# Optimization experiments

Hardware: AMD Instinct MI355X
Metric: run time of the kernel (lower is better)

## Reference

```python
import jax, jax.numpy as jnp
import numpy as np
from jax.ops import segment_sum, segment_max

N_USERS = 50000
N_ITEMS = 30000
N_ENTITIES = 80000
D = 64
KG_HOPS = 2        # context_hops / KG_layers
LGCN_LAYERS = 2    # n_layers
TEMP = 0.2
N_KG_EDGES = 2_000_000
N_INTERACT = 1_000_000
N_ADJ = 2_000_000
EPS_PD = 1e-6      # torch PairwiseDistance default eps


def _normalize(x):
    # F.normalize(x, p=2, dim=-1)
    n = jnp.linalg.norm(x, axis=-1, keepdims=True)
    return x / jnp.clip(n, 1e-12)


def _spmm(rows, cols, vals, x, n_rows):
    # sparse (n_rows x k) @ dense (k x d) via gather + segment_sum
    return segment_sum(vals[:, None] * x[cols], rows, num_segments=n_rows)


def setup_inputs() -> dict:
    key = jax.random.key(0)
    ks = jax.random.split(key, 9)
    all_embed = jax.random.normal(ks[0], (N_USERS + N_ENTITIES, D), dtype=jnp.float32) * 0.1
    interact_vals = jax.random.uniform(ks[1], (N_INTERACT,), dtype=jnp.float32)
    adj_vals = jax.random.uniform(ks[2], (N_ADJ,), dtype=jnp.float32)
    edge_index = jax.random.randint(ks[3], (2, N_KG_EDGES), 0, N_ENTITIES, dtype=jnp.int32)
    edge_type = jax.random.randint(ks[4], (N_KG_EDGES,), 0, 32, dtype=jnp.int32)
    interact_rows = jnp.sort(jax.random.randint(ks[5], (N_INTERACT,), 0, N_USERS, dtype=jnp.int32))
    interact_cols = jax.random.randint(ks[6], (N_INTERACT,), 0, N_ITEMS, dtype=jnp.int32)
    adj_rows = jax.random.randint(ks[7], (N_ADJ,), 0, N_USERS + N_ITEMS, dtype=jnp.int32)
    adj_cols = jax.random.randint(ks[8], (N_ADJ,), 0, N_USERS + N_ITEMS, dtype=jnp.int32)
    return {
        "all_embed": all_embed,
        "interact_vals": interact_vals,
        "adj_vals": adj_vals,
        "edge_index": edge_index,
        "edge_type": edge_type,
        "interact_rows": interact_rows,
        "interact_cols": interact_cols,
        "adj_rows": adj_rows,
        "adj_cols": adj_cols,
    }


def _forward(all_embed, interact_vals, adj_vals, edge_index, interact_rows,
             interact_cols, adj_rows, adj_cols):
    user_emb = all_embed[:N_USERS]
    entity_emb = all_embed[N_USERS:]
    head, tail = edge_index[0], edge_index[1]

    u_res, e_res = user_emb, entity_emb
    u, e = user_emb, entity_emb
    ones = jnp.ones((head.shape[0],), dtype=entity_emb.dtype)
    cnt = jnp.clip(segment_sum(ones, head, num_segments=N_ENTITIES), 1.0)

    for _ in range(KG_HOPS):
        # scatter_mean KG aggregation: entity_agg[h] = mean over tails of edges with head h
        entity_agg = segment_sum(e[tail], head, num_segments=N_ENTITIES) / cnt[:, None]
        item_agg = entity_agg[:N_ITEMS]
        # user_mean = interact_map @ entity_agg[:n_items]
        user_mean = _spmm(interact_rows, interact_cols, interact_vals, item_agg, N_USERS)
        # pairwise L2 distance per interaction nnz
        diff = item_agg[interact_cols] - user_mean[interact_rows] + EPS_PD
        score = jnp.linalg.norm(diff, axis=-1) / TEMP
        # sparse softmax over rows (users)
        m = segment_max(score, interact_rows, num_segments=N_USERS)
        ex = jnp.exp(score - m[interact_rows])
        denom = segment_sum(ex, interact_rows, num_segments=N_USERS)
        att = ex / denom[interact_rows]
        # user_agg = sparse.mm(soft_score_mat, item_agg)
        user_agg = segment_sum(att[:, None] * item_agg[interact_cols],
                               interact_rows, num_segments=N_USERS)
        e = _normalize(entity_agg)
        u = _normalize(user_agg)
        e_res = e_res + e
        u_res = u_res + u

    # LightGCN over bipartite graph
    x = jnp.concatenate([u_res, e_res[:N_ITEMS]], axis=0)  # [n_users+n_items, D]
    acc = x
    for _ in range(LGCN_LAYERS):
        x = _spmm(adj_rows, adj_cols, adj_vals, x, N_USERS + N_ITEMS)
        acc = acc + x
    out = acc / float(LGCN_LAYERS + 1)
    return out[:N_USERS], out[N_USERS:]


def reference(all_embed, interact_vals, adj_vals, edge_index, edge_type,
              interact_rows, interact_cols, adj_rows, adj_cols):
    # edge_type is passed through the original forward but unused by Aggregator
    return _forward(all_embed, interact_vals, adj_vals, edge_index,
                    interact_rows, interact_cols, adj_rows, adj_cols)
```

## Files before the change

kernel.cpp:

```cpp
#include <hip/hip_runtime.h>
#include <math.h>

#define N_USERS 50000
#define N_ITEMS 30000
#define N_ENTITIES 80000
#define N_UI (N_USERS + N_ITEMS)
#define D 64
#define N_KG_EDGES 2000000
#define N_INTERACT 1000000
#define N_ADJ 2000000
#define INV_TEMP 5.0f
#define EPS_PD 1e-6f
#define SHIFT 7
#define NB 625
#define BKEYS 128
#define BMASK 127
#define EPB 8192
#define BIG 1024
#define GRID_EP 245
#define UH_GRID 12500
#define KG2_GRID 7500
#define CVT_GRID 1875

typedef _Float16 f16;

__device__ __forceinline__ float4 ld_h4(const f16* p) {
    struct h4 { f16 x, y, z, w; };
    h4 h = *(const h4*)p;
    return make_float4((float)h.x, (float)h.y, (float)h.z, (float)h.w);
}

__device__ __forceinline__ void st_h4(f16* p, float4 v) {
    struct h4 { f16 x, y, z, w; };
    h4 h = {(f16)v.x, (f16)v.y, (f16)v.z, (f16)v.w};
    *(h4*)p = h;
}

__global__ void bhist_plus(const int* __restrict__ kg_ei, const int* __restrict__ adj_r,
                           const int* __restrict__ irows, int* __restrict__ bcntK,
                           int* __restrict__ bcntA, int* __restrict__ rowstart) {
    __shared__ int h[NB];
    int bb = blockIdx.x;
    if (bb < 2 * GRID_EP) {
        bool kg = bb < GRID_EP;
        const int* keys = kg ? kg_ei : adj_r;
        int* bcnt = kg ? bcntK : bcntA;
        int blk = kg ? bb : bb - GRID_EP;
        int n = kg ? N_KG_EDGES : N_ADJ;
        for (int i = threadIdx.x; i < NB; i += BIG) h[i] = 0;
        __syncthreads();
        int e0 = blk * EPB, e1 = min(e0 + EPB, n);
        for (int e = e0 + (int)threadIdx.x; e < e1; e += BIG)
            atomicAdd(&h[keys[e] >> SHIFT], 1);
        __syncthreads();
        for (int i = threadIdx.x; i < NB; i += BIG)
            if (h[i]) atomicAdd(&bcnt[i], h[i]);
    } else {
        int r = (bb - 2 * GRID_EP) * BIG + threadIdx.x;
        if (r > N_USERS) return;
        int lo = 0, hi = N_INTERACT;
        while (lo < hi) {
            int mid = (lo + hi) >> 1;
            if (irows[mid] < r) lo = mid + 1; else hi = mid;
        }
        rowstart[r] = lo;
    }
}

__global__ void bscan_both(const int* __restrict__ cntK, int* __restrict__ boffK,
                           int* __restrict__ bcurK, const int* __restrict__ cntA,
                           int* __restrict__ boffA, int* __restrict__ bcurA) {
    __shared__ int wp[4];
    __shared__ int carry_s;
    const int* cnt = blockIdx.x ? cntA : cntK;
    int* boff = blockIdx.x ? boffA : boffK;
    int* bcur = blockIdx.x ? bcurA : bcurK;
    int lane = threadIdx.x & 63, wv = threadIdx.x >> 6;
    if (threadIdx.x == 0) { carry_s = 0; boff[0] = 0; }
    __syncthreads();
    for (int base = 0; base < NB; base += 256) {
        int i = base + (int)threadIdx.x;
        int v = (i < NB) ? cnt[i] : 0;
        int x = v;
        #pragma unroll
        for (int o = 1; o < 64; o <<= 1) {
            int t = __shfl_up(x, o, 64);
            if (lane >= o) x += t;
        }
        if (lane == 63) wp[wv] = x;
        __syncthreads();
        int add = carry_s;
        for (int j = 0; j < wv; ++j) add += wp[j];
        int incl = x + add;
        if (i < NB) { boff[i + 1] = incl; bcur[i] = incl - v; }
        __syncthreads();
        if (threadIdx.x == 255) carry_s = incl;
        __syncthreads();
    }
}

__global__ void binA_both(const int* __restrict__ kg_ei, int* __restrict__ bcurK,
                          int* __restrict__ kg_bin, const int* __restrict__ adj_r,
                          const int* __restrict__ adj_c, const float* __restrict__ adj_v,
                          int* __restrict__ bcurA, int2* __restrict__ rc) {
    __shared__ int hist[NB], base[NB];
    bool kg = blockIdx.x < GRID_EP;
    int blk = kg ? blockIdx.x : blockIdx.x - GRID_EP;
    int n = kg ? N_KG_EDGES : N_ADJ;
    int* bcur = kg ? bcurK : bcurA;
    const int* keys = kg ? kg_ei : adj_r;
    for (int i = threadIdx.x; i < NB; i += BIG) hist[i] = 0;
    __syncthreads();
    int e0 = blk * EPB;
    for (int i = threadIdx.x; i < EPB; i += BIG) {
        int e = e0 + i;
        if (e < n) atomicAdd(&hist[keys[e] >> SHIFT], 1);
    }
    __syncthreads();
    for (int b = threadIdx.x; b < NB; b += BIG)
        base[b] = hist[b] ? atomicAdd(&bcur[b], hist[b]) : 0;
    __syncthreads();
    for (int i = threadIdx.x; i < NB; i += BIG) hist[i] = 0;
    __syncthreads();
    for (int i = threadIdx.x; i < EPB; i += BIG) {
        int e = e0 + i;
        if (e >= n) continue;
        int k = keys[e];
        int b = k >> SHIFT;
        int slot = base[b] + atomicAdd(&hist[b], 1);
        if (kg) kg_bin[slot] = (kg_ei[n + e] << SHIFT) | (k & BMASK);
        else    rc[slot] = make_int2((adj_c[e] << SHIFT) | (k & BMASK),
                                     __float_as_int(adj_v[e]));
    }
}

__global__ void binC_both(const int* __restrict__ boffK, const int* __restrict__ kg_bin,
                          int* __restrict__ tails, int* __restrict__ rowptrK,
                          float* __restrict__ icnt, const int* __restrict__ boffA,
                          const int2* __restrict__ rc, int2* __restrict__ pair,
                          int* __restrict__ rowptrA) {
    __shared__ int cnt_s[BKEYS];
    __shared__ int cur_s[BKEYS];
    __shared__ int wp2[2];
    bool kg = blockIdx.x < NB;
    int b = kg ? blockIdx.x : blockIdx.x - NB;
    const int* boff = kg ? boffK : boffA;
    int k0 = b << SHIFT;
    int s = boff[b], t = boff[b + 1];
    if (threadIdx.x < BKEYS) cnt_s[threadIdx.x] = 0;
    __syncthreads();
    for (int i = s + (int)threadIdx.x; i < t; i += 256)
        atomicAdd(&cnt_s[(kg ? kg_bin[i] : rc[i].x) & BMASK], 1);
    __syncthreads();
    int lane = threadIdx.x & 63, wv = threadIdx.x >> 6;
    int v = (threadIdx.x < BKEYS) ? cnt_s[threadIdx.x] : 0;
    int x = v;
    #pragma unroll
    for (int o = 1; o < 64; o <<= 1) {
        int tt = __shfl_up(x, o, 64);
        if (lane >= o) x += tt;
    }
    if (threadIdx.x < BKEYS && lane == 63) wp2[wv] = x;
    __syncthreads();
    int add = (wv == 1) ? wp2[0] : 0;
    int excl = s + (x - v) + add;
    if (threadIdx.x < BKEYS) {
        cur_s[threadIdx.x] = excl;
        if (kg) {
            rowptrK[k0 + threadIdx.x] = excl;
            icnt[k0 + threadIdx.x] = 1.0f / fmaxf((float)v, 1.0f);
        } else {
            rowptrA[k0 + threadIdx.x] = excl;
        }
    }
    if (threadIdx.x == 0 && b == NB - 1) {
        if (kg) rowptrK[N_ENTITIES] = t; else rowptrA[N_UI] = t;
    }
    __syncthreads();
    if (kg) {
        for (int i = s + (int)threadIdx.x; i < t; i += 256) {
            int p = kg_bin[i];
            int slot = atomicAdd(&cur_s[p & BMASK], 1);
            tails[slot] = (unsigned)p >> SHIFT;
        }
    } else {
        for (int i = s + (int)threadIdx.x; i < t; i += 256) {
            int2 p = rc[i];
            int slot = atomicAdd(&cur_s[p.x & BMASK], 1);
            pair[slot] = make_int2((unsigned)p.x >> SHIFT, p.y);
        }
    }
}

template <bool FIRST>
__device__ __forceinline__ void kg_hop_body(
        int wid, const int* __restrict__ rowptr, const int* __restrict__ tails,
        const float* __restrict__ icnt, const float* __restrict__ Ain,
        float* __restrict__ Aout, float* __restrict__ ER,
        const float* __restrict__ ERI, float* __restrict__ snorm, int nrows) {
    int lane = threadIdx.x & 63;
    int g = lane >> 4, gl = lane & 15;
    if (wid >= nrows) return;
    int s = rowptr[wid], t = rowptr[wid + 1];
    float4 acc = {0.f, 0.f, 0.f, 0.f};
    for (int e = s + g; e < t; e += 16) {
        int e1 = e + 4, e2 = e + 8, e3 = e + 12;
        int c0 = tails[e];
        int c1 = (e1 < t) ? tails[e1] : 0;
        int c2 = (e2 < t) ? tails[e2] : 0;
        int c3 = (e3 < t) ? tails[e3] : 0;
        float4 r0 = *(const float4*)(Ain + (size_t)c0 * D + gl * 4);
        float4 r1 = {0.f, 0.f, 0.f, 0.f};
        float4 r2 = {0.f, 0.f, 0.f, 0.f};
        float4 r3 = {0.f, 0.f, 0.f, 0.f};
        if (e1 < t) r1 = *(const float4*)(Ain + (size_t)c1 * D + gl * 4);
        if (e2 < t) r2 = *(const float4*)(Ain + (size_t)c2 * D + gl * 4);
        if (e3 < t) r3 = *(const float4*)(Ain + (size_t)c3 * D + gl * 4);
        acc.x += (r0.x + r1.x) + (r2.x + r3.x);
        acc.y += (r0.y + r1.y) + (r2.y + r3.y);
        acc.z += (r0.z + r1.z) + (r2.z + r3.z);
        acc.w += (r0.w + r1.w) + (r2.w + r3.w);
    }
    acc.x += __shfl_xor(acc.x, 16, 64); acc.x += __shfl_xor(acc.x, 32, 64);
    acc.y += __shfl_xor(acc.y, 16, 64); acc.y += __shfl_xor(acc.y, 32, 64);
    acc.z += __shfl_xor(acc.z, 16, 64); acc.z += __shfl_xor(acc.z, 32, 64);
    acc.w += __shfl_xor(acc.w, 16, 64); acc.w += __shfl_xor(acc.w, 32, 64);
    float ss = acc.x * acc.x + acc.y * acc.y + acc.z * acc.z + acc.w * acc.w;
    ss += __shfl_xor(ss, 1, 64); ss += __shfl_xor(ss, 2, 64);
    ss += __shfl_xor(ss, 4, 64); ss += __shfl_xor(ss, 8, 64);
    float nrm = fmaxf(sqrtf(ss), 1e-12f);
    float inv = 1.0f / nrm;
    if (g == 0) {
        size_t o = (size_t)wid * D + gl * 4;
        float4 ev = {acc.x * inv, acc.y * inv, acc.z * inv, acc.w * inv};
        *(float4*)(Aout + o) = ev;
        if (wid < N_ITEMS) {
            float4 er = FIRST ? *(const float4*)(ERI + o) : *(const float4*)(ER + o);
            er.x += ev.x; er.y += ev.y; er.z += ev.z; er.w += ev.w;
            *(float4*)(ER + o) = er;
            if (gl == 0) snorm[wid] = nrm * icnt[wid];
        }
    }
}

template <bool FIRST>
__device__ __forceinline__ void user_hop_body(
        int wid, const float* __restrict__ E, const float* __restrict__ snorm,
        const int* __restrict__ rowstart, const int* __restrict__ cols,
        const float* __restrict__ vals, float* __restrict__ UR,
        const float* __restrict__ URI, f16* __restrict__ XHu) {
    int lane = threadIdx.x & 63;
    int g = lane >> 4, gl = lane & 15;
    if (wid >= N_USERS) return;
    int s = rowstart[wid], t = rowstart[wid + 1];

    float4 mean = {0.f, 0.f, 0.f, 0.f};
    #define UH_LOAD(K)                                                          \
        const int eP##K = s + g + 4 * K;                                        \
        const bool ok##K = eP##K < t;                                           \
        const int cP##K = ok##K ? cols[eP##K] : 0;                              \
        const float snP##K = ok##K ? snorm[cP##K] : 0.f;                        \
        const float vP##K = ok##K ? vals[eP##K] : 0.f;                          \
        float4 rP##K = {0.f, 0.f, 0.f, 0.f};                                    \
        if (ok##K) rP##K = *(const float4*)(E + (size_t)cP##K * D + gl * 4);
    UH_LOAD(0) UH_LOAD(1) UH_LOAD(2) UH_LOAD(3) UH_LOAD(4) UH_LOAD(5)
    #undef UH_LOAD
    #define UH_MEAN(K) {                                                        \
        float w = vP##K * snP##K;                                               \
        mean.x += w * rP##K.x; mean.y += w * rP##K.y;                           \
        mean.z += w * rP##K.z; mean.w += w * rP##K.w; }
    UH_MEAN(0) UH_MEAN(1) UH_MEAN(2) UH_MEAN(3) UH_MEAN(4) UH_MEAN(5)
    #undef UH_MEAN
    for (int e = s + g + 24; e < t; e += 4) {
        int c = cols[e];
        float w = vals[e] * snorm[c];
        float4 r = *(const float4*)(E + (size_t)c * D + gl * 4);
        mean.x += w * r.x; mean.y += w * r.y;
        mean.z += w * r.z; mean.w += w * r.w;
    }
    mean.x += __shfl_xor(mean.x, 16, 64); mean.x += __shfl_xor(mean.x, 32, 64);
    mean.y += __shfl_xor(mean.y, 16, 64); mean.y += __shfl_xor(mean.y, 32, 64);
    mean.z += __shfl_xor(mean.z, 16, 64); mean.z += __shfl_xor(mean.z, 32, 64);
    mean.w += __shfl_xor(mean.w, 16, 64); mean.w += __shfl_xor(mean.w, 32, 64);

    float m = -INFINITY, denom = 0.f;
    float4 acc = {0.f, 0.f, 0.f, 0.f};
    #define UH_SM(K) if (ok##K) {                                               \
        float4 il = {snP##K * rP##K.x, snP##K * rP##K.y,                        \
                     snP##K * rP##K.z, snP##K * rP##K.w};                       \
        float dx = il.x - mean.x + EPS_PD;                                      \
        float dy = il.y - mean.y + EPS_PD;                                      \
        float dz = il.z - mean.z + EPS_PD;                                      \
        float dw = il.w - mean.w + EPS_PD;                                      \
        float ssl = dx * dx + dy * dy + dz * dz + dw * dw;                      \
        ssl += __shfl_xor(ssl, 1, 64); ssl += __shfl_xor(ssl, 2, 64);           \
        ssl += __shfl_xor(ssl, 4, 64); ssl += __shfl_xor(ssl, 8, 64);           \
        float sc = sqrtf(ssl) * INV_TEMP;                                       \
        float m_new = fmaxf(m, sc);                                             \
        float scale = __expf(m - m_new);                                        \
        float ex = __expf(sc - m_new);                                          \
        denom = denom * scale + ex;                                             \
        acc.x = acc.x * scale + ex * il.x;                                      \
        acc.y = acc.y * scale + ex * il.y;                                      \
        acc.z = acc.z * scale + ex * il.z;                                      \
        acc.w = acc.w * scale + ex * il.w;                                      \
        m = m_new; }
    UH_SM(0) UH_SM(1) UH_SM(2) UH_SM(3) UH_SM(4) UH_SM(5)
    #undef UH_SM
    for (int e = s + g + 24; e < t; e += 4) {
        int c = cols[e];
        float sn = snorm[c];
        float4 r = *(const float4*)(E + (size_t)c * D + gl * 4);
        float4 il = {sn * r.x, sn * r.y, sn * r.z, sn * r.w};
        float dx = il.x - mean.x + EPS_PD;
        float dy = il.y - mean.y + EPS_PD;
        float dz = il.z - mean.z + EPS_PD;
        float dw = il.w - mean.w + EPS_PD;
        float ssl = dx * dx + dy * dy + dz * dz + dw * dw;
        ssl += __shfl_xor(ssl, 1, 64); ssl += __shfl_xor(ssl, 2, 64);
        ssl += __shfl_xor(ssl, 4, 64); ssl += __shfl_xor(ssl, 8, 64);
        float sc = sqrtf(ssl) * INV_TEMP;
        float m_new = fmaxf(m, sc);
        float scale = __expf(m - m_new);
        float ex = __expf(sc - m_new);
        denom = denom * scale + ex;
        acc.x = acc.x * scale + ex * il.x;
        acc.y = acc.y * scale + ex * il.y;
        acc.z = acc.z * scale + ex * il.z;
        acc.w = acc.w * scale + ex * il.w;
        m = m_new;
    }
    float mg = fmaxf(m, __shfl_xor(m, 16, 64));
    mg = fmaxf(mg, __shfl_xor(mg, 32, 64));
    float scl = __expf(fmaxf(m - mg, -88.0f));
    denom *= scl;
    acc.x *= scl; acc.y *= scl; acc.z *= scl; acc.w *= scl;
    denom += __shfl_xor(denom, 16, 64); denom += __shfl_xor(denom, 32, 64);
    acc.x += __shfl_xor(acc.x, 16, 64); acc.x += __shfl_xor(acc.x, 32, 64);
    acc.y += __shfl_xor(acc.y, 16, 64); acc.y += __shfl_xor(acc.y, 32, 64);
    acc.z += __shfl_xor(acc.z, 16, 64); acc.z += __shfl_xor(acc.z, 32, 64);
    acc.w += __shfl_xor(acc.w, 16, 64); acc.w += __shfl_xor(acc.w, 32, 64);
    float invd = denom > 0.f ? 1.0f / denom : 0.f;
    acc.x *= invd; acc.y *= invd; acc.z *= invd; acc.w *= invd;
    float ss = acc.x * acc.x + acc.y * acc.y + acc.z * acc.z + acc.w * acc.w;
    ss += __shfl_xor(ss, 1, 64); ss += __shfl_xor(ss, 2, 64);
    ss += __shfl_xor(ss, 4, 64); ss += __shfl_xor(ss, 8, 64);
    float inv = 1.0f / fmaxf(sqrtf(ss), 1e-12f);
    if (g == 0) {
        size_t o = (size_t)wid * D + gl * 4;
        float4 u = FIRST ? *(const float4*)(URI + o) : *(const float4*)(UR + o);
        u.x += acc.x * inv; u.y += acc.y * inv; u.z += acc.z * inv; u.w += acc.w * inv;
        *(float4*)(UR + o) = u;
        if (XHu) st_h4(XHu + o, u);
    }
}

__global__ void kg1_kernel(const int* __restrict__ rowptr, const int* __restrict__ tails,
                           const float* __restrict__ icnt, const float* __restrict__ Ain,
                           float* __restrict__ A1, float* __restrict__ ER,
                           const float* __restrict__ ERI, float* __restrict__ sn1) {
    int wid = (blockIdx.x * blockDim.x + threadIdx.x) >> 6;
    kg_hop_body<true>(wid, rowptr, tails, icnt, Ain, A1, ER, ERI, sn1, N_ENTITIES);
}

__global__ void mid_kernel(const float* __restrict__ A1, const float* __restrict__ sn1,
                           const int* __restrict__ rowstart, const int* __restrict__ cols,
                           const float* __restrict__ vals, float* __restrict__ UR,
                           const float* __restrict__ URI, const int* __restrict__ rowptr,
                           const int* __restrict__ tails, const float* __restrict__ icnt,
                           float* __restrict__ A0I, float* __restrict__ ER,
                           float* __restrict__ sn2) {
    if (blockIdx.x < UH_GRID) {
        int wid = (blockIdx.x * blockDim.x + threadIdx.x) >> 6;
        user_hop_body<true>(wid, A1, sn1, rowstart, cols, vals, UR, URI, nullptr);
    } else {
        int wid = (((blockIdx.x - UH_GRID) * blockDim.x) + threadIdx.x) >> 6;
        kg_hop_body<false>(wid, rowptr, tails, icnt, A1, A0I, ER, nullptr, sn2, N_ITEMS);
    }
}

__global__ void fin_kernel(const float* __restrict__ A0I, const float* __restrict__ sn2,
                           const int* __restrict__ rowstart, const int* __restrict__ cols,
                           const float* __restrict__ vals, float* __restrict__ UR,
                           f16* __restrict__ XH, const float* __restrict__ ER) {
    if (blockIdx.x < UH_GRID) {
        int wid = (blockIdx.x * blockDim.x + threadIdx.x) >> 6;
        user_hop_body<false>(wid, A0I, sn2, rowstart, cols, vals, UR, nullptr, XH);
    } else {
        int i = (blockIdx.x - UH_GRID) * blockDim.x + threadIdx.x;
        if (i < (N_ITEMS * D) / 4)
            st_h4(XH + (size_t)N_USERS * D + (size_t)i * 4,
                  *(const float4*)(ER + (size_t)i * 4));
    }
}

__device__ __forceinline__ const float* xrow32(const float* U, const float* I, int c) {
    return (c < N_USERS) ? (U + (size_t)c * D) : (I + (size_t)(c - N_USERS) * D);
}

template <int MODE>
__global__ void adj_spmm(const int* __restrict__ rowptr, const int2* __restrict__ pair,
                         const f16* __restrict__ X, const float* __restrict__ XAU,
                         const float* __restrict__ XAI, f16* __restrict__ Y,
                         float* __restrict__ out) {
    int wid = (blockIdx.x * blockDim.x + threadIdx.x) >> 6;
    int lane = threadIdx.x & 63;
    int g = lane >> 4, gl = lane & 15;
    if (wid >= N_UI) return;
    int s = rowptr[wid], t = rowptr[wid + 1];
    float4 acc = {0.f, 0.f, 0.f, 0.f};
    for (int e = s + g; e < t; e += 16) {
        int e1 = e + 4, e2 = e + 8, e3 = e + 12;
        int2 p0 = pair[e];
        int2 p1 = (e1 < t) ? pair[e1] : make_int2(0, 0);
        int2 p2 = (e2 < t) ? pair[e2] : make_int2(0, 0);
        int2 p3 = (e3 < t) ? pair[e3] : make_int2(0, 0);
        float4 r0 = ld_h4(X + (size_t)p0.x * D + gl * 4);
        float4 r1 = {0.f, 0.f, 0.f, 0.f};
        float4 r2 = {0.f, 0.f, 0.f, 0.f};
        float4 r3 = {0.f, 0.f, 0.f, 0.f};
        if (e1 < t) r1 = ld_h4(X + (size_t)p1.x * D + gl * 4);
        if (e2 < t) r2 = ld_h4(X + (size_t)p2.x * D + gl * 4);
        if (e3 < t) r3 = ld_h4(X + (size_t)p3.x * D + gl * 4);
        float v0 = __int_as_float(p0.y), v1 = __int_as_float(p1.y);
        float v2 = __int_as_float(p2.y), v3 = __int_as_float(p3.y);
        acc.x += (v0 * r0.x + v1 * r1.x) + (v2 * r2.x + v3 * r3.x);
        acc.y += (v0 * r0.y + v1 * r1.y) + (v2 * r2.y + v3 * r3.y);
        acc.z += (v0 * r0.z + v1 * r1.z) + (v2 * r2.z + v3 * r3.z);
        acc.w += (v0 * r0.w + v1 * r1.w) + (v2 * r2.w + v3 * r3.w);
    }
    acc.x += __shfl_xor(acc.x, 16, 64); acc.x += __shfl_xor(acc.x, 32, 64);
    acc.y += __shfl_xor(acc.y, 16, 64); acc.y += __shfl_xor(acc.y, 32, 64);
    acc.z += __shfl_xor(acc.z, 16, 64); acc.z += __shfl_xor(acc.z, 32, 64);
    acc.w += __shfl_xor(acc.w, 16, 64); acc.w += __shfl_xor(acc.w, 32, 64);
    if (g == 0) {
        size_t o = (size_t)wid * D + gl * 4;
        if (MODE == 0) {
            st_h4(Y + o, acc);
            const float4 xa = *(const float4*)(xrow32(XAU, XAI, wid) + gl * 4);
            float4 ov = {xa.x + acc.x, xa.y + acc.y, xa.z + acc.z, xa.w + acc.w};
            *(float4*)(out + o) = ov;
        } else {
            float4 ov = *(const float4*)(out + o);
            ov.x = (ov.x + acc.x) * (1.0f / 3.0f);
            ov.y = (ov.y + acc.y) * (1.0f / 3.0f);
            ov.z = (ov.z + acc.z) * (1.0f / 3.0f);
            ov.w = (ov.w + acc.w) * (1.0f / 3.0f);
            *(float4*)(out + o) = ov;
        }
    }
}

extern "C" void kernel_launch(void* const* d_in, const int* in_sizes, int n_in,
                              void* d_out, int out_size, void* d_ws, size_t ws_size,
                              hipStream_t stream) {
    const float* all_embed     = (const float*)d_in[0];
    const float* interact_vals = (const float*)d_in[1];
    const float* adj_vals      = (const float*)d_in[2];
    const int*   edge_index    = (const int*)d_in[3];
    const int*   interact_rows = (const int*)d_in[5];
    const int*   interact_cols = (const int*)d_in[6];
    const int*   adj_rows      = (const int*)d_in[7];
    const int*   adj_cols      = (const int*)d_in[8];
    float* out = (float*)d_out;

    const size_t usrN = (size_t)N_USERS * D;
    const size_t itmN = (size_t)N_ITEMS * D;
    const size_t entN = (size_t)N_ENTITIES * D;

    float* cur = (float*)d_ws;
    float* UR  = cur; cur += usrN;
    float* ER  = cur; cur += itmN;
    float* A0I = cur; cur += itmN;
    float* A1  = cur; cur += entN;
    int* KG_TAIL = (int*)cur; cur += N_KG_EDGES;
    int2* ADJ_PAIR = (int2*)cur; cur += 2 * (size_t)N_ADJ;
    float* ICNT   = cur; cur += N_ENTITIES;
    float* SNORM1 = cur; cur += N_ITEMS + 16;
    float* SNORM2 = cur; cur += N_ITEMS + 16;
    int* KG_ROWPTR  = (int*)cur;
    int* ADJ_ROWPTR = KG_ROWPTR + N_ENTITIES + 2;
    int* BCNT_K     = ADJ_ROWPTR + N_UI + 2;
    int* BCNT_A     = BCNT_K + NB;
    int* BOFF_K     = BCNT_A + NB;
    int* BOFF_A     = BOFF_K + NB + 1;
    int* BCUR_K     = BOFF_A + NB + 1;
    int* BCUR_A     = BCUR_K + NB;
    int* ROWSTART   = BCUR_A + NB;

    int*  KG_BIN = (int*)UR;
    int2* ADJ_RC = (int2*)A1;
    f16*  XH  = (f16*)A1;
    f16*  X1H = XH + (size_t)N_UI * D;

    hipMemsetAsync(BCNT_K, 0, 2 * NB * sizeof(int), stream);
    bhist_plus<<<2 * GRID_EP + 49, BIG, 0, stream>>>(edge_index, adj_rows, interact_rows,
                                                     BCNT_K, BCNT_A, ROWSTART);
    bscan_both<<<2, 256, 0, stream>>>(BCNT_K, BOFF_K, BCUR_K, BCNT_A, BOFF_A, BCUR_A);
    binA_both<<<2 * GRID_EP, BIG, 0, stream>>>(edge_index, BCUR_K, KG_BIN, adj_rows,
                                               adj_cols, adj_vals, BCUR_A, ADJ_RC);
    binC_both<<<2 * NB, 256, 0, stream>>>(BOFF_K, KG_BIN, KG_TAIL, KG_ROWPTR, ICNT,
                                          BOFF_A, ADJ_RC, ADJ_PAIR, ADJ_ROWPTR);

    kg1_kernel<<<N_ENTITIES / 4, 256, 0, stream>>>(KG_ROWPTR, KG_TAIL, ICNT,
                                                   all_embed + usrN, A1, ER,
                                                   all_embed + usrN, SNORM1);
    mid_kernel<<<UH_GRID + KG2_GRID, 256, 0, stream>>>(A1, SNORM1, ROWSTART,
                                                       interact_cols, interact_vals,
                                                       UR, all_embed, KG_ROWPTR, KG_TAIL,
                                                       ICNT, A0I, ER, SNORM2);
    fin_kernel<<<UH_GRID + CVT_GRID, 256, 0, stream>>>(A0I, SNORM2, ROWSTART,
                                                       interact_cols, interact_vals,
                                                       UR, XH, ER);

    adj_spmm<0><<<N_UI / 4, 256, 0, stream>>>(ADJ_ROWPTR, ADJ_PAIR, XH, UR, ER, X1H, out);
    adj_spmm<1><<<N_UI / 4, 256, 0, stream>>>(ADJ_ROWPTR, ADJ_PAIR, X1H, nullptr, nullptr,
                                              nullptr, out);
}
```

Before: 415.2 us.

## Overlap adjacency binning with KG hops, pack adj pairs, simplify softmax distance

The adjacency binning passes move out of the standalone bin kernels and into kg1 and mid as extra blocks, so they run alongside the KG and user hop work. Adjacency (col, val) pairs are packed into one 32-bit word holding a 17-bit column and a 15-bit fp16 value with the sign bit dropped. This halves edge-stream traffic in both SpMM passes. The user-hop distance is expanded algebraically into a dot product against a precomputed (mean - eps) vector, and the online softmax is changed to use a single exp per edge. Blocks grow to 1024 threads. The packing relies on non-negative values and assumes the rescaled weights stay within fp16 precision.

```diff
diff --git a/kernel.cpp b/kernel.cpp
--- a/kernel.cpp
+++ b/kernel.cpp
@@ -18,11 +18,13 @@
 #define EPB 8192
 #define BIG 1024
 #define GRID_EP 245
-#define UH_GRID 12500
-#define KG2_GRID 7500
-#define CVT_GRID 1875
+#define KG1_G 5000
+#define UH_G 3125
+#define KG2_G 1875
+#define CVT_G 469
 
 typedef _Float16 f16;
+typedef unsigned short u16;
 
 __device__ __forceinline__ float4 ld_h4(const f16* p) {
     struct h4 { f16 x, y, z, w; };
@@ -36,9 +38,18 @@
     *(h4*)p = h;
 }
 
-__global__ void bhist_plus(const int* __restrict__ kg_ei, const int* __restrict__ adj_r,
-                           const int* __restrict__ irows, int* __restrict__ bcntK,
-                           int* __restrict__ bcntA, int* __restrict__ rowstart) {
+__device__ __forceinline__ u16 f16_bits(float v) {
+    f16 h = (f16)v;
+    return __builtin_bit_cast(u16, h);
+}
+
+__device__ __forceinline__ float bits_f16(unsigned b) {
+    return (float)__builtin_bit_cast(f16, (u16)b);
+}
+
+__global__ void stageA(const int* __restrict__ kg_ei, const int* __restrict__ adj_r,
+                       const int* __restrict__ irows, int* __restrict__ bcntK,
+                       int* __restrict__ bcntA, int* __restrict__ rowstart) {
     __shared__ int h[NB];
     int bb = blockIdx.x;
     if (bb < 2 * GRID_EP) {
@@ -99,22 +110,15 @@
     }
 }
 
-__global__ void binA_both(const int* __restrict__ kg_ei, int* __restrict__ bcurK,
-                          int* __restrict__ kg_bin, const int* __restrict__ adj_r,
-                          const int* __restrict__ adj_c, const float* __restrict__ adj_v,
-                          int* __restrict__ bcurA, int2* __restrict__ rc) {
+__global__ void binA_kg(const int* __restrict__ ei, int* __restrict__ bcur,
+                        int* __restrict__ binned) {
     __shared__ int hist[NB], base[NB];
-    bool kg = blockIdx.x < GRID_EP;
-    int blk = kg ? blockIdx.x : blockIdx.x - GRID_EP;
-    int n = kg ? N_KG_EDGES : N_ADJ;
-    int* bcur = kg ? bcurK : bcurA;
-    const int* keys = kg ? kg_ei : adj_r;
     for (int i = threadIdx.x; i < NB; i += BIG) hist[i] = 0;
     __syncthreads();
-    int e0 = blk * EPB;
+    int e0 = blockIdx.x * EPB;
     for (int i = threadIdx.x; i < EPB; i += BIG) {
         int e = e0 + i;
-        if (e < n) atomicAdd(&hist[keys[e] >> SHIFT], 1);
+        if (e < N_KG_EDGES) atomicAdd(&hist[ei[e] >> SHIFT], 1);
     }
     __syncthreads();
     for (int b = threadIdx.x; b < NB; b += BIG)
@@ -124,33 +128,27 @@
     __syncthreads();
     for (int i = threadIdx.x; i < EPB; i += BIG) {
         int e = e0 + i;
-        if (e >= n) continue;
-        int k = keys[e];
+        if (e >= N_KG_EDGES) continue;
+        int k = ei[e];
         int b = k >> SHIFT;
         int slot = base[b] + atomicAdd(&hist[b], 1);
-        if (kg) kg_bin[slot] = (kg_ei[n + e] << SHIFT) | (k & BMASK);
-        else    rc[slot] = make_int2((adj_c[e] << SHIFT) | (k & BMASK),
-                                     __float_as_int(adj_v[e]));
-    }
-}
-
-__global__ void binC_both(const int* __restrict__ boffK, const int* __restrict__ kg_bin,
-                          int* __restrict__ tails, int* __restrict__ rowptrK,
-                          float* __restrict__ icnt, const int* __restrict__ boffA,
-                          const int2* __restrict__ rc, int2* __restrict__ pair,
-                          int* __restrict__ rowptrA) {
+        binned[slot] = (ei[N_KG_EDGES + e] << SHIFT) | (k & BMASK);
+    }
+}
+
+__global__ void binC_kg(const int* __restrict__ boff, const int* __restrict__ binned,
+                        int* __restrict__ tails, int* __restrict__ rowptr,
+                        float* __restrict__ icnt) {
     __shared__ int cnt_s[BKEYS];
     __shared__ int cur_s[BKEYS];
     __shared__ int wp2[2];
-    bool kg = blockIdx.x < NB;
-    int b = kg ? blockIdx.x : blockIdx.x - NB;
-    const int* boff = kg ? boffK : boffA;
+    int b = blockIdx.x;
     int k0 = b << SHIFT;
     int s = boff[b], t = boff[b + 1];
     if (threadIdx.x < BKEYS) cnt_s[threadIdx.x] = 0;
     __syncthreads();
-    for (int i = s + (int)threadIdx.x; i < t; i += 256)
-        atomicAdd(&cnt_s[(kg ? kg_bin[i] : rc[i].x) & BMASK], 1);
+    for (int i = s + (int)threadIdx.x; i < t; i += BIG)
+        atomicAdd(&cnt_s[binned[i] & BMASK], 1);
     __syncthreads();
     int lane = threadIdx.x & 63, wv = threadIdx.x >> 6;
     int v = (threadIdx.x < BKEYS) ? cnt_s[threadIdx.x] : 0;
@@ -166,29 +164,15 @@
     int excl = s + (x - v) + add;
     if (threadIdx.x < BKEYS) {
         cur_s[threadIdx.x] = excl;
-        if (kg) {
-            rowptrK[k0 + threadIdx.x] = excl;
-            icnt[k0 + threadIdx.x] = 1.0f / fmaxf((float)v, 1.0f);
-        } else {
-            rowptrA[k0 + threadIdx.x] = excl;
-        }
-    }
-    if (threadIdx.x == 0 && b == NB - 1) {
-        if (kg) rowptrK[N_ENTITIES] = t; else rowptrA[N_UI] = t;
-    }
-    __syncthreads();
-    if (kg) {
-        for (int i = s + (int)threadIdx.x; i < t; i += 256) {
-            int p = kg_bin[i];
-            int slot = atomicAdd(&cur_s[p & BMASK], 1);
-            tails[slot] = (unsigned)p >> SHIFT;
-        }
-    } else {
-        for (int i = s + (int)threadIdx.x; i < t; i += 256) {
-            int2 p = rc[i];
-            int slot = atomicAdd(&cur_s[p.x & BMASK], 1);
-            pair[slot] = make_int2((unsigned)p.x >> SHIFT, p.y);
-        }
+        rowptr[k0 + threadIdx.x] = excl;
+        icnt[k0 + threadIdx.x] = 1.0f / fmaxf((float)v, 1.0f);
+    }
+    if (threadIdx.x == 0 && b == NB - 1) rowptr[N_ENTITIES] = t;
+    __syncthreads();
+    for (int i = s + (int)threadIdx.x; i < t; i += BIG) {
+        int p = binned[i];
+        int slot = atomicAdd(&cur_s[p & BMASK], 1);
+        tails[slot] = (unsigned)p >> SHIFT;
     }
 }
 
@@ -283,52 +267,54 @@
     mean.z += __shfl_xor(mean.z, 16, 64); mean.z += __shfl_xor(mean.z, 32, 64);
     mean.w += __shfl_xor(mean.w, 16, 64); mean.w += __shfl_xor(mean.w, 32, 64);
 
+    float4 b = {mean.x - EPS_PD, mean.y - EPS_PD, mean.z - EPS_PD, mean.w - EPS_PD};
+    float bb = b.x * b.x + b.y * b.y + b.z * b.z + b.w * b.w;
+    bb += __shfl_xor(bb, 1, 64); bb += __shfl_xor(bb, 2, 64);
+    bb += __shfl_xor(bb, 4, 64); bb += __shfl_xor(bb, 8, 64);
+
     float m = -INFINITY, denom = 0.f;
     float4 acc = {0.f, 0.f, 0.f, 0.f};
     #define UH_SM(K) if (ok##K) {                                               \
-        float4 il = {snP##K * rP##K.x, snP##K * rP##K.y,                        \
-                     snP##K * rP##K.z, snP##K * rP##K.w};                       \
-        float dx = il.x - mean.x + EPS_PD;                                      \
-        float dy = il.y - mean.y + EPS_PD;                                      \
-        float dz = il.z - mean.z + EPS_PD;                                      \
-        float dw = il.w - mean.w + EPS_PD;                                      \
-        float ssl = dx * dx + dy * dy + dz * dz + dw * dw;                      \
-        ssl += __shfl_xor(ssl, 1, 64); ssl += __shfl_xor(ssl, 2, 64);           \
-        ssl += __shfl_xor(ssl, 4, 64); ssl += __shfl_xor(ssl, 8, 64);           \
-        float sc = sqrtf(ssl) * INV_TEMP;                                       \
-        float m_new = fmaxf(m, sc);                                             \
-        float scale = __expf(m - m_new);                                        \
-        float ex = __expf(sc - m_new);                                          \
+        float dl = rP##K.x * b.x + rP##K.y * b.y + rP##K.z * b.z + rP##K.w * b.w; \
+        dl += __shfl_xor(dl, 1, 64); dl += __shfl_xor(dl, 2, 64);               \
+        dl += __shfl_xor(dl, 4, 64); dl += __shfl_xor(dl, 8, 64);               \
+        float s2 = fmaxf(snP##K * snP##K - 2.f * snP##K * dl + bb, 0.f);        \
+        float sc = sqrtf(s2) * INV_TEMP;                                        \
+        float dlt = sc - m;                                                     \
+        float tt = __expf(fminf(dlt, -dlt));                                    \
+        bool up = dlt > 0.f;                                                    \
+        float scale = up ? tt : 1.f;                                            \
+        float ex = up ? 1.f : tt;                                               \
+        if (up) m = sc;                                                         \
         denom = denom * scale + ex;                                             \
-        acc.x = acc.x * scale + ex * il.x;                                      \
-        acc.y = acc.y * scale + ex * il.y;                                      \
-        acc.z = acc.z * scale + ex * il.z;                                      \
-        acc.w = acc.w * scale + ex * il.w;                                      \
-        m = m_new; }
+        float w = ex * snP##K;                                                  \
+        acc.x = acc.x * scale + w * rP##K.x;                                    \
+        acc.y = acc.y * scale + w * rP##K.y;                                    \
+        acc.z = acc.z * scale + w * rP##K.z;                                    \
+        acc.w = acc.w * scale + w * rP##K.w; }
     UH_SM(0) UH_SM(1) UH_SM(2) UH_SM(3) UH_SM(4) UH_SM(5)
     #undef UH_SM
     for (int e = s + g + 24; e < t; e += 4) {
         int c = cols[e];
         float sn = snorm[c];
         float4 r = *(const float4*)(E + (size_t)c * D + gl * 4);
-        float4 il = {sn * r.x, sn * r.y, sn * r.z, sn * r.w};
-        float dx = il.x - mean.x + EPS_PD;
-        float dy = il.y - mean.y + EPS_PD;
-        float dz = il.z - mean.z + EPS_PD;
-        float dw = il.w - mean.w + EPS_PD;
-        float ssl = dx * dx + dy * dy + dz * dz + dw * dw;
-        ssl += __shfl_xor(ssl, 1, 64); ssl += __shfl_xor(ssl, 2, 64);
-        ssl += __shfl_xor(ssl, 4, 64); ssl += __shfl_xor(ssl, 8, 64);
-        float sc = sqrtf(ssl) * INV_TEMP;
-        float m_new = fmaxf(m, sc);
-        float scale = __expf(m - m_new);
-        float ex = __expf(sc - m_new);
+        float dl = r.x * b.x + r.y * b.y + r.z * b.z + r.w * b.w;
+        dl += __shfl_xor(dl, 1, 64); dl += __shfl_xor(dl, 2, 64);
+        dl += __shfl_xor(dl, 4, 64); dl += __shfl_xor(dl, 8, 64);
+        float s2 = fmaxf(sn * sn - 2.f * sn * dl + bb, 0.f);
+        float sc = sqrtf(s2) * INV_TEMP;
+        float dlt = sc - m;
+        float tt = __expf(fminf(dlt, -dlt));
+        bool up = dlt > 0.f;
+        float scale = up ? tt : 1.f;
+        float ex = up ? 1.f : tt;
+        if (up) m = sc;
         denom = denom * scale + ex;
-        acc.x = acc.x * scale + ex * il.x;
-        acc.y = acc.y * scale + ex * il.y;
-        acc.z = acc.z * scale + ex * il.z;
-        acc.w = acc.w * scale + ex * il.w;
-        m = m_new;
+        float w = ex * sn;
+        acc.x = acc.x * scale + w * r.x;
+        acc.y = acc.y * scale + w * r.y;
+        acc.z = acc.z * scale + w * r.z;
+        acc.w = acc.w * scale + w * r.w;
     }
     float mg = fmaxf(m, __shfl_xor(m, 16, 64));
     mg = fmaxf(mg, __shfl_xor(mg, 32, 64));
@@ -355,12 +341,42 @@
     }
 }
 
-__global__ void kg1_kernel(const int* __restrict__ rowptr, const int* __restrict__ tails,
-                           const float* __restrict__ icnt, const float* __restrict__ Ain,
-                           float* __restrict__ A1, float* __restrict__ ER,
-                           const float* __restrict__ ERI, float* __restrict__ sn1) {
-    int wid = (blockIdx.x * blockDim.x + threadIdx.x) >> 6;
-    kg_hop_body<true>(wid, rowptr, tails, icnt, Ain, A1, ER, ERI, sn1, N_ENTITIES);
+__global__ void kg1_binA(const int* __restrict__ rowptr, const int* __restrict__ tails,
+                         const float* __restrict__ icnt, const float* __restrict__ Ain,
+                         float* __restrict__ A1, float* __restrict__ ER,
+                         const float* __restrict__ ERI, float* __restrict__ sn1,
+                         const int* __restrict__ adj_r, const int* __restrict__ adj_c,
+                         const float* __restrict__ adj_v, int* __restrict__ bcurA,
+                         int* __restrict__ rcx, u16* __restrict__ rcv) {
+    if (blockIdx.x < KG1_G) {
+        int wid = (blockIdx.x * BIG + threadIdx.x) >> 6;
+        kg_hop_body<true>(wid, rowptr, tails, icnt, Ain, A1, ER, ERI, sn1, N_ENTITIES);
+    } else {
+        __shared__ int hist[NB], base[NB];
+        int blk = blockIdx.x - KG1_G;
+        for (int i = threadIdx.x; i < NB; i += BIG) hist[i] = 0;
+        __syncthreads();
+        int e0 = blk * EPB;
+        for (int i = threadIdx.x; i < EPB; i += BIG) {
+            int e = e0 + i;
+            if (e < N_ADJ) atomicAdd(&hist[adj_r[e] >> SHIFT], 1);
+        }
+        __syncthreads();
+        for (int b = threadIdx.x; b < NB; b += BIG)
+            base[b] = hist[b] ? atomicAdd(&bcurA[b], hist[b]) : 0;
+        __syncthreads();
+        for (int i = threadIdx.x; i < NB; i += BIG) hist[i] = 0;
+        __syncthreads();
+        for (int i = threadIdx.x; i < EPB; i += BIG) {
+            int e = e0 + i;
+            if (e >= N_ADJ) continue;
+            int r = adj_r[e];
+            int b = r >> SHIFT;
+            int slot = base[b] + atomicAdd(&hist[b], 1);
+            rcx[slot] = (adj_c[e] << SHIFT) | (r & BMASK);
+            rcv[slot] = f16_bits(adj_v[e]);
+        }
+    }
 }
 
 __global__ void mid_kernel(const float* __restrict__ A1, const float* __restrict__ sn1,
@@ -369,13 +385,50 @@
                            const float* __restrict__ URI, const int* __restrict__ rowptr,
                            const int* __restrict__ tails, const float* __restrict__ icnt,
                            float* __restrict__ A0I, float* __restrict__ ER,
-                           float* __restrict__ sn2) {
-    if (blockIdx.x < UH_GRID) {
-        int wid = (blockIdx.x * blockDim.x + threadIdx.x) >> 6;
+                           float* __restrict__ sn2, const int* __restrict__ boffA,
+                           const int* __restrict__ rcx, const u16* __restrict__ rcv,
+                           int* __restrict__ pair, int* __restrict__ rowptrA) {
+    if (blockIdx.x < UH_G) {
+        int wid = (blockIdx.x * BIG + threadIdx.x) >> 6;
         user_hop_body<true>(wid, A1, sn1, rowstart, cols, vals, UR, URI, nullptr);
+    } else if (blockIdx.x < UH_G + KG2_G) {
+        int wid = ((blockIdx.x - UH_G) * BIG + threadIdx.x) >> 6;
+        kg_hop_body<false>(wid, rowptr, tails, icnt, A1, A0I, ER, nullptr, sn2, N_ITEMS);
     } else {
-        int wid = (((blockIdx.x - UH_GRID) * blockDim.x) + threadIdx.x) >> 6;
-        kg_hop_body<false>(wid, rowptr, tails, icnt, A1, A0I, ER, nullptr, sn2, N_ITEMS);
+        __shared__ int cnt_s[BKEYS];
+        __shared__ int cur_s[BKEYS];
+        __shared__ int wp2[2];
+        int b = blockIdx.x - (UH_G + KG2_G);
+        int k0 = b << SHIFT;
+        int s = boffA[b], t = boffA[b + 1];
+        if (threadIdx.x < BKEYS) cnt_s[threadIdx.x] = 0;
+        __syncthreads();
+        for (int i = s + (int)threadIdx.x; i < t; i += BIG)
+            atomicAdd(&cnt_s[rcx[i] & BMASK], 1);
+        __syncthreads();
+        int lane = threadIdx.x & 63, wv = threadIdx.x >> 6;
+        int v = (threadIdx.x < BKEYS) ? cnt_s[threadIdx.x] : 0;
+        int x = v;
+        #pragma unroll
+        for (int o = 1; o < 64; o <<= 1) {
+            int tt = __shfl_up(x, o, 64);
+            if (lane >= o) x += tt;
+        }
+        if (threadIdx.x < BKEYS && lane == 63) wp2[wv] = x;
+        __syncthreads();
+        int add = (wv == 1) ? wp2[0] : 0;
+        int excl = s + (x - v) + add;
+        if (threadIdx.x < BKEYS) {
+            cur_s[threadIdx.x] = excl;
+            rowptrA[k0 + threadIdx.x] = excl;
+        }
+        if (threadIdx.x == 0 && b == NB - 1) rowptrA[N_UI] = t;
+        __syncthreads();
+        for (int i = s + (int)threadIdx.x; i < t; i += BIG) {
+            int p = rcx[i];
+            int slot = atomicAdd(&cur_s[p & BMASK], 1);
+            pair[slot] = (int)(((unsigned)p >> SHIFT << 15) | (rcv[i] & 0x7FFFu));
+        }
     }
 }
 
@@ -383,11 +436,11 @@
                            const int* __restrict__ rowstart, const int* __restrict__ cols,
                            const float* __restrict__ vals, float* __restrict__ UR,
                            f16* __restrict__ XH, const float* __restrict__ ER) {
-    if (blockIdx.x < UH_GRID) {
-        int wid = (blockIdx.x * blockDim.x + threadIdx.x) >> 6;
+    if (blockIdx.x < UH_G) {
+        int wid = (blockIdx.x * BIG + threadIdx.x) >> 6;
         user_hop_body<false>(wid, A0I, sn2, rowstart, cols, vals, UR, nullptr, XH);
     } else {
-        int i = (blockIdx.x - UH_GRID) * blockDim.x + threadIdx.x;
+        int i = (blockIdx.x - UH_G) * BIG + threadIdx.x;
         if (i < (N_ITEMS * D) / 4)
             st_h4(XH + (size_t)N_USERS * D + (size_t)i * 4,
                   *(const float4*)(ER + (size_t)i * 4));
@@ -399,11 +452,11 @@
 }
 
 template <int MODE>
-__global__ void adj_spmm(const int* __restrict__ rowptr, const int2* __restrict__ pair,
+__global__ void adj_spmm(const int* __restrict__ rowptr, const int* __restrict__ pair,
                          const f16* __restrict__ X, const float* __restrict__ XAU,
                          const float* __restrict__ XAI, f16* __restrict__ Y,
                          float* __restrict__ out) {
-    int wid = (blockIdx.x * blockDim.x + threadIdx.x) >> 6;
+    int wid = (blockIdx.x * BIG + threadIdx.x) >> 6;
     int lane = threadIdx.x & 63;
     int g = lane >> 4, gl = lane & 15;
     if (wid >= N_UI) return;
@@ -411,19 +464,22 @@
     float4 acc = {0.f, 0.f, 0.f, 0.f};
     for (int e = s + g; e < t; e += 16) {
         int e1 = e + 4, e2 = e + 8, e3 = e + 12;
-        int2 p0 = pair[e];
-        int2 p1 = (e1 < t) ? pair[e1] : make_int2(0, 0);
-        int2 p2 = (e2 < t) ? pair[e2] : make_int2(0, 0);
-        int2 p3 = (e3 < t) ? pair[e3] : make_int2(0, 0);
-        float4 r0 = ld_h4(X + (size_t)p0.x * D + gl * 4);
+        int p0 = pair[e];
+        int p1 = (e1 < t) ? pair[e1] : 0;
+        int p2 = (e2 < t) ? pair[e2] : 0;
+        int p3 = (e3 < t) ? pair[e3] : 0;
+        float4 r0 = ld_h4(X + (size_t)((unsigned)p0 >> 15) * D + gl * 4);
         float4 r1 = {0.f, 0.f, 0.f, 0.f};
         float4 r2 = {0.f, 0.f, 0.f, 0.f};
         float4 r3 = {0.f, 0.f, 0.f, 0.f};
-        if (e1 < t) r1 = ld_h4(X + (size_t)p1.x * D + gl * 4);
-        if (e2 < t) r2 = ld_h4(X + (size_t)p2.x * D + gl * 4);
-        if (e3 < t) r3 = ld_h4(X + (size_t)p3.x * D + gl * 4);
-        float v0 = __int_as_float(p0.y), v1 = __int_as_float(p1.y);
-        float v2 = __int_as_float(p2.y), v3 = __int_as_float(p3.y);
+        if (e1 < t) r1 = ld_h4(X + (size_t)((unsigned)p1 >> 15) * D + gl * 4);
+        if (e2 < t) r2 = ld_h4(X + (size_t)((unsigned)p2 >> 15) * D + gl * 4);
+        if (e3 < t) r3 = ld_h4(X + (size_t)((unsigned)p3 >> 15) * D + gl * 4);
+        float v0 = bits_f16(p0 & 0x7FFF), v1 = bits_f16(p1 & 0x7FFF);
+        float v2 = bits_f16(p2 & 0x7FFF), v3 = bits_f16(p3 & 0x7FFF);
+        if (e1 >= t) v1 = 0.f;
+        if (e2 >= t) v2 = 0.f;
+        if (e3 >= t) v3 = 0.f;
         acc.x += (v0 * r0.x + v1 * r1.x) + (v2 * r2.x + v3 * r3.x);
         acc.y += (v0 * r0.y + v1 * r1.y) + (v2 * r2.y + v3 * r3.y);
         acc.z += (v0 * r0.z + v1 * r1.z) + (v2 * r2.z + v3 * r3.z);
@@ -473,8 +529,10 @@
     float* ER  = cur; cur += itmN;
     float* A0I = cur; cur += itmN;
     float* A1  = cur; cur += entN;
-    int* KG_TAIL = (int*)cur; cur += N_KG_EDGES;
-    int2* ADJ_PAIR = (int2*)cur; cur += 2 * (size_t)N_ADJ;
+    int*  KG_TAIL = (int*)cur;  cur += N_KG_EDGES;
+    int*  ADJ_RCX = (int*)cur;  cur += N_ADJ;
+    u16*  ADJ_RCV = (u16*)cur;  cur += N_ADJ / 2;
+    int*  ADJ_PAIR = (int*)cur; cur += N_ADJ;
     float* ICNT   = cur; cur += N_ENTITIES;
     float* SNORM1 = cur; cur += N_ITEMS + 16;
     float* SNORM2 = cur; cur += N_ITEMS + 16;
@@ -488,32 +546,32 @@
     int* BCUR_A     = BCUR_K + NB;
     int* ROWSTART   = BCUR_A + NB;
 
-    int*  KG_BIN = (int*)UR;
-    int2* ADJ_RC = (int2*)A1;
-    f16*  XH  = (f16*)A1;
-    f16*  X1H = XH + (size_t)N_UI * D;
+    int* KG_BIN = (int*)UR;
+    f16* XH  = (f16*)A1;
+    f16* X1H = XH + (size_t)N_UI * D;
 
     hipMemsetAsync(BCNT_K, 0, 2 * NB * sizeof(int), stream);
-    bhist_plus<<<2 * GRID_EP + 49, BIG, 0, stream>>>(edge_index, adj_rows, interact_rows,
-                                                     BCNT_K, BCNT_A, ROWSTART);
+    stageA<<<2 * GRID_EP + 49, BIG, 0, stream>>>(edge_index, adj_rows, interact_rows,
+                                                 BCNT_K, BCNT_A, ROWSTART);
     bscan_both<<<2, 256, 0, stream>>>(BCNT_K, BOFF_K, BCUR_K, BCNT_A, BOFF_A, BCUR_A);
-    binA_both<<<2 * GRID_EP, BIG, 0, stream>>>(edge_index, BCUR_K, KG_BIN, adj_rows,
-                                               adj_cols, adj_vals, BCUR_A, ADJ_RC);
-    binC_both<<<2 * NB, 256, 0, stream>>>(BOFF_K, KG_BIN, KG_TAIL, KG_ROWPTR, ICNT,
-                                          BOFF_A, ADJ_RC, ADJ_PAIR, ADJ_ROWPTR);
-
-    kg1_kernel<<<N_ENTITIES / 4, 256, 0, stream>>>(KG_ROWPTR, KG_TAIL, ICNT,
-                                                   all_embed + usrN, A1, ER,
-                                                   all_embed + usrN, SNORM1);
-    mid_kernel<<<UH_GRID + KG2_GRID, 256, 0, stream>>>(A1, SNORM1, ROWSTART,
-                                                       interact_cols, interact_vals,
-                                                       UR, all_embed, KG_ROWPTR, KG_TAIL,
-                                                       ICNT, A0I, ER, SNORM2);
-    fin_kernel<<<UH_GRID + CVT_GRID, 256, 0, stream>>>(A0I, SNORM2, ROWSTART,
-                                                       interact_cols, interact_vals,
-                                                       UR, XH, ER);
-
-    adj_spmm<0><<<N_UI / 4, 256, 0, stream>>>(ADJ_ROWPTR, ADJ_PAIR, XH, UR, ER, X1H, out);
-    adj_spmm<1><<<N_UI / 4, 256, 0, stream>>>(ADJ_ROWPTR, ADJ_PAIR, X1H, nullptr, nullptr,
-                                              nullptr, out);
-}
+    binA_kg<<<GRID_EP, BIG, 0, stream>>>(edge_index, BCUR_K, KG_BIN);
+    binC_kg<<<NB, BIG, 0, stream>>>(BOFF_K, KG_BIN, KG_TAIL, KG_ROWPTR, ICNT);
+
+    kg1_binA<<<KG1_G + GRID_EP, BIG, 0, stream>>>(KG_ROWPTR, KG_TAIL, ICNT,
+                                                  all_embed + usrN, A1, ER,
+                                                  all_embed + usrN, SNORM1,
+                                                  adj_rows, adj_cols, adj_vals,
+                                                  BCUR_A, ADJ_RCX, ADJ_RCV);
+    mid_kernel<<<UH_G + KG2_G + NB, BIG, 0, stream>>>(A1, SNORM1, ROWSTART,
+                                                      interact_cols, interact_vals,
+                                                      UR, all_embed, KG_ROWPTR, KG_TAIL,
+                                                      ICNT, A0I, ER, SNORM2, BOFF_A,
+                                                      ADJ_RCX, ADJ_RCV, ADJ_PAIR,
+                                                      ADJ_ROWPTR);
+    fin_kernel<<<UH_G + CVT_G, BIG, 0, stream>>>(A0I, SNORM2, ROWSTART, interact_cols,
+                                                 interact_vals, UR, XH, ER);
+
+    adj_spmm<0><<<KG1_G, BIG, 0, stream>>>(ADJ_ROWPTR, ADJ_PAIR, XH, UR, ER, X1H, out);
+    adj_spmm<1><<<KG1_G, BIG, 0, stream>>>(ADJ_ROWPTR, ADJ_PAIR, X1H, nullptr, nullptr,
+                                           nullptr, out);
+}
```

Result: slower. 441.8 us (+6.4%).
